# Optimization experiments

Measured on AMD Instinct MI355X. Metric: run time of the kernel, lower is better.

Reference implementation:

```python
import jax, jax.numpy as jnp
import numpy as np


def _gru(ub, lengths, W_ih, W_hh, b_ih, b_hh, h0):
    # ub: [B,T,E] pooled basket sequence; emulates packed GRU + pad_packed:
    # hidden carries forward only while t < length; outputs are zero past length.
    B, T, E = ub.shape
    x_t = jnp.transpose(ub, (1, 0, 2))                      # [T,B,E]
    mask_t = (jnp.arange(T)[:, None] < lengths[None, :])    # [T,B]
    xg_t = x_t @ W_ih.T + b_ih                              # [T,B,3E] precompute input gates

    def step(h, inp):
        xg, m = inp                                         # [B,3E], [B]
        hg = h @ W_hh.T + b_hh                              # [B,3E]
        xr, xz, xn = jnp.split(xg, 3, axis=-1)
        hr, hz, hn = jnp.split(hg, 3, axis=-1)
        r = jax.nn.sigmoid(xr + hr)
        z = jax.nn.sigmoid(xz + hz)
        n = jnp.tanh(xn + r * hn)
        h_new = (1.0 - z) * n + z * h
        m = m[:, None]
        h_next = jnp.where(m, h_new, h)
        out = jnp.where(m, h_new, 0.0)                      # pad_packed pads with zeros
        return h_next, out

    h_last, outs = jax.lax.scan(step, h0[0], (xg_t, mask_t))
    dynamic_user = jnp.transpose(outs, (1, 0, 2))           # [B,T,E]
    return dynamic_user, h_last[None]                        # h_u: [1,B,E]


def setup_inputs() -> dict:
    key = jax.random.key(0)
    B, T, M, E, V = 256, 50, 20, 128, 100000
    ks = jax.random.split(key, 8)
    basket_sizes = jax.random.randint(ks[0], (B, T), 1, M + 1)
    item_ids = jax.random.randint(ks[1], (B, T, M), 1, V + 2)
    pos = jnp.arange(M)
    item_ids = jnp.where(pos[None, None, :] < basket_sizes[..., None], item_ids, 0)
    lengths = jnp.sort(jax.random.randint(ks[2], (B,), 1, T + 1))[::-1]  # descending, like pack_padded
    emb = jax.random.normal(ks[3], (V + 2, E), jnp.float32) * 0.1
    emb = emb.at[0].set(0.0)                                 # padding_idx=0
    s = 1.0 / np.sqrt(E)
    W_ih = jax.random.uniform(ks[4], (3 * E, E), jnp.float32, -s, s)
    W_hh = jax.random.uniform(ks[5], (3 * E, E), jnp.float32, -s, s)
    b_ih = jax.random.uniform(ks[6], (3 * E,), jnp.float32, -s, s)
    b_hh = jax.random.uniform(ks[7], (3 * E,), jnp.float32, -s, s)
    h0 = jnp.zeros((1, B, E), jnp.float32)
    return {"item_ids": item_ids, "basket_sizes": basket_sizes, "lengths": lengths,
            "emb": emb, "W_ih": W_ih, "W_hh": W_hh, "b_ih": b_ih, "b_hh": b_hh, "h0": h0}


def reference(item_ids, basket_sizes, lengths, emb, W_ih, W_hh, b_ih, b_hh, h0):
    # Fused ragged embedding-bag (avg): row 0 of emb is zero, so padded slots
    # contribute nothing; divide by true basket size -> exact avg pool over basket.
    gathered = emb[item_ids]                                 # [B,T,M,E]
    ub_seqs = gathered.sum(axis=2) / basket_sizes[..., None].astype(gathered.dtype)  # [B,T,E]
    dynamic_user, h_u = _gru(ub_seqs, lengths, W_ih, W_hh, b_ih, b_hh, h0)
    return dynamic_user, h_u
```

## Files before the change

### kernel.cpp

```cpp
#include <hip/hip_runtime.h>
#include <stdint.h>

#define Bn 256
#define Tn 50
#define Mn 20
#define En 128
#define G3 384
#define MT 64
#define LDA 132

__device__ __forceinline__ float sigmoidf(float x) {
    return 1.0f / (1.0f + __expf(-x));
}
__device__ __forceinline__ float tanh_safe(float a) {
    float ax = fabsf(a);
    float e2 = __expf(-2.0f * ax);
    return copysignf((1.0f - e2) / (1.0f + e2), a);
}

__global__ __launch_bounds__(256) void gather_kernel(
    const int*   __restrict__ item_ids,
    const int*   __restrict__ basket_sizes,
    const float* __restrict__ emb,
    float* __restrict__ ub)
{
    const int bt   = blockIdx.x * 8 + (threadIdx.x >> 5);
    const int lane = threadIdx.x & 31;
    const int* ids = item_ids + (size_t)bt * Mn;
    float ax = 0.f, ay = 0.f, az = 0.f, aw = 0.f;
    #pragma unroll
    for (int m = 0; m < Mn; ++m) {
        const float4 v = *(const float4*)(emb + (size_t)ids[m] * En + lane * 4);
        ax += v.x; ay += v.y; az += v.z; aw += v.w;
    }
    const float inv = 1.0f / (float)basket_sizes[bt];
    *(float4*)(ub + (size_t)bt * En + lane * 4) =
        make_float4(ax * inv, ay * inv, az * inv, aw * inv);
}

__global__ __launch_bounds__(256, 2) void gemm_kernel(
    const float* __restrict__ ub,
    const float* __restrict__ W_ih,
    const float* __restrict__ b_ih,
    float* __restrict__ xg)
{
    __shared__ float A[MT][LDA];
    __shared__ float Bt[64][LDA];

    const int tid  = threadIdx.x;
    const int mt   = blockIdx.x / 6;
    const int nc   = blockIdx.x % 6;
    const int row0 = mt * MT;
    const int col0 = nc * 64;

    {
        const int r = tid >> 2, seg = tid & 3;
        const float4* srcA = (const float4*)(ub + (size_t)(row0 + r) * En + seg * 32);
        const float4* srcB = (const float4*)(W_ih + (size_t)(col0 + r) * En + seg * 32);
        float4* dstA = (float4*)&A[r][seg * 32];
        float4* dstB = (float4*)&Bt[r][seg * 32];
        #pragma unroll
        for (int c = 0; c < 8; ++c) { dstA[c] = srcA[c]; dstB[c] = srcB[c]; }
    }
    __syncthreads();

    const int tx = tid & 15;
    const int ty = tid >> 4;

    float acc[4][4];
    #pragma unroll
    for (int i = 0; i < 4; ++i)
        #pragma unroll
        for (int u = 0; u < 4; ++u) acc[i][u] = 0.0f;

    #pragma unroll 4
    for (int k4 = 0; k4 < 32; ++k4) {
        const float4 av[4] = {
            *(const float4*)&A[ty +  0][k4*4], *(const float4*)&A[ty + 16][k4*4],
            *(const float4*)&A[ty + 32][k4*4], *(const float4*)&A[ty + 48][k4*4]};
        const float4 bv[4] = {
            *(const float4*)&Bt[tx +  0][k4*4], *(const float4*)&Bt[tx + 16][k4*4],
            *(const float4*)&Bt[tx + 32][k4*4], *(const float4*)&Bt[tx + 48][k4*4]};
        #pragma unroll
        for (int i = 0; i < 4; ++i)
            #pragma unroll
            for (int u = 0; u < 4; ++u) {
                acc[i][u] = fmaf(av[i].x, bv[u].x, acc[i][u]);
                acc[i][u] = fmaf(av[i].y, bv[u].y, acc[i][u]);
                acc[i][u] = fmaf(av[i].z, bv[u].z, acc[i][u]);
                acc[i][u] = fmaf(av[i].w, bv[u].w, acc[i][u]);
            }
    }

    float bias[4];
    #pragma unroll
    for (int u = 0; u < 4; ++u) bias[u] = b_ih[col0 + tx + 16*u];
    #pragma unroll
    for (int i = 0; i < 4; ++i) {
        const size_t rowoff = (size_t)(row0 + ty + 16*i) * G3;
        #pragma unroll
        for (int u = 0; u < 4; ++u)
            xg[rowoff + col0 + tx + 16*u] = acc[i][u] + bias[u];
    }
}

__global__ __launch_bounds__(1024) void gru_kernel(
    const int*   __restrict__ lengths,
    const float* __restrict__ W_hh,
    const float* __restrict__ b_hh,
    const float* __restrict__ h0,
    const float* __restrict__ xg,
    float* __restrict__ out_dyn,
    float* __restrict__ out_h)
{
    __shared__ float hs[En];
    __shared__ float red[8][3][En];

    const int tid = threadIdx.x;
    const int b   = blockIdx.x;
    const int j   = tid & 127;
    const int q   = tid >> 7;

    float4 w0[4], w1[4], w2[4];
    {
        const float4* p0 = (const float4*)(W_hh + (size_t)(0*En + j) * En + q * 16);
        const float4* p1 = (const float4*)(W_hh + (size_t)(1*En + j) * En + q * 16);
        const float4* p2 = (const float4*)(W_hh + (size_t)(2*En + j) * En + q * 16);
        #pragma unroll
        for (int c = 0; c < 4; ++c) { w0[c] = p0[c]; w1[c] = p1[c]; w2[c] = p2[c]; }
    }

    const int len = lengths[b];
    const float* xgb = xg + (size_t)b * Tn * G3;
    float* outb = out_dyn + (size_t)b * Tn * En;

    float xr = 0.f, xz = 0.f, xn = 0.f, br = 0.f, bz = 0.f, bn = 0.f;
    if (tid < En) {
        hs[tid] = h0[(size_t)b * En + tid];
        br = b_hh[tid]; bz = b_hh[En + tid]; bn = b_hh[2*En + tid];
        xr = xgb[tid];  xz = xgb[En + tid]; xn = xgb[2*En + tid];
    }
    __syncthreads();

    for (int t = 0; t < len; ++t) {
        const float4* h4 = ((const float4*)hs) + q * 4;
        float a0 = 0.f, a1 = 0.f, a2 = 0.f;
        #pragma unroll
        for (int c = 0; c < 4; ++c) {
            const float4 hv = h4[c];
            a0 = fmaf(w0[c].x, hv.x, a0); a0 = fmaf(w0[c].y, hv.y, a0);
            a0 = fmaf(w0[c].z, hv.z, a0); a0 = fmaf(w0[c].w, hv.w, a0);
            a1 = fmaf(w1[c].x, hv.x, a1); a1 = fmaf(w1[c].y, hv.y, a1);
            a1 = fmaf(w1[c].z, hv.z, a1); a1 = fmaf(w1[c].w, hv.w, a1);
            a2 = fmaf(w2[c].x, hv.x, a2); a2 = fmaf(w2[c].y, hv.y, a2);
            a2 = fmaf(w2[c].z, hv.z, a2); a2 = fmaf(w2[c].w, hv.w, a2);
        }
        red[q][0][j] = a0; red[q][1][j] = a1; red[q][2][j] = a2;

        float nxr = 0.f, nxz = 0.f, nxn = 0.f;
        if (tid < En) {
            const int tn = (t + 1 < len) ? t + 1 : t;
            nxr = xgb[tn*G3 + tid];
            nxz = xgb[tn*G3 + En + tid];
            nxn = xgb[tn*G3 + 2*En + tid];
        }
        __syncthreads();

        if (tid < En) {
            float ar = red[0][0][tid], az = red[0][1][tid], an = red[0][2][tid];
            #pragma unroll
            for (int p = 1; p < 8; ++p) {
                ar += red[p][0][tid]; az += red[p][1][tid]; an += red[p][2][tid];
            }
            const float r = sigmoidf(xr + br + ar);
            const float z = sigmoidf(xz + bz + az);
            const float n = tanh_safe(xn + r * (bn + an));
            const float hnew = (1.0f - z) * n + z * hs[tid];
            hs[tid] = hnew;
            outb[t*En + tid] = hnew;
            xr = nxr; xz = nxz; xn = nxn;
        }
        __syncthreads();
    }

    if (tid < En) {
        for (int t = len; t < Tn; ++t) outb[t*En + tid] = 0.0f;
        out_h[(size_t)b * En + tid] = hs[tid];
    }
}

extern "C" void kernel_launch(void* const* d_in, const int* in_sizes, int n_in,
                              void* d_out, int out_size, void* d_ws, size_t ws_size,
                              hipStream_t stream) {
    const int*   item_ids     = (const int*)d_in[0];
    const int*   basket_sizes = (const int*)d_in[1];
    const int*   lengths      = (const int*)d_in[2];
    const float* emb          = (const float*)d_in[3];
    const float* W_ih         = (const float*)d_in[4];
    const float* W_hh         = (const float*)d_in[5];
    const float* b_ih         = (const float*)d_in[6];
    const float* b_hh         = (const float*)d_in[7];
    const float* h0           = (const float*)d_in[8];
    float* out = (float*)d_out;
    float* xg  = (float*)d_ws;
    float* ub  = out;

    gather_kernel<<<(Bn * Tn) / 8, 256, 0, stream>>>(item_ids, basket_sizes, emb, ub);
    gemm_kernel<<<1200, 256, 0, stream>>>(ub, W_ih, b_ih, xg);
    gru_kernel<<<Bn, 1024, 0, stream>>>(
        lengths, W_hh, b_hh, h0, xg, out, out + (size_t)Bn * Tn * En);
}
```

Before: 176.5 us.

## Restructure GRU recurrence to use shuffle reductions and double-buffered hidden state

The GRU kernel now uses 512 threads per batch row. Each group of 4 adjacent lanes splits the K dimension for one hidden unit and reduces with wavefront shuffles instead of shared-memory partial sums. The hidden state is double-buffered in shared memory, so each timestep needs one barrier instead of two. Gate math is computed redundantly by all 4 lanes, and the weight rows rotate their chunk order to reduce LDS bank conflicts. Each thread now holds twice as many weight registers (96 floats), which may pressure occupancy despite the launch bound of 2.

Result: no change. 176.5 us (+0.0%).

```diff
diff --git a/kernel.cpp b/kernel.cpp
--- a/kernel.cpp
+++ b/kernel.cpp
@@ -104,7 +104,7 @@
     }
 }
 
-__global__ __launch_bounds__(1024) void gru_kernel(
+__global__ __launch_bounds__(512, 2) void gru_kernel(
     const int*   __restrict__ lengths,
     const float* __restrict__ W_hh,
     const float* __restrict__ b_hh,
@@ -113,41 +113,42 @@
     float* __restrict__ out_dyn,
     float* __restrict__ out_h)
 {
-    __shared__ float hs[En];
-    __shared__ float red[8][3][En];
+    __shared__ float hs[2][En];
 
     const int tid = threadIdx.x;
     const int b   = blockIdx.x;
-    const int j   = tid & 127;
-    const int q   = tid >> 7;
-
-    float4 w0[4], w1[4], w2[4];
+    const int j   = tid >> 2;
+    const int q   = tid & 3;
+
+    float4 w0[8], w1[8], w2[8];
     {
-        const float4* p0 = (const float4*)(W_hh + (size_t)(0*En + j) * En + q * 16);
-        const float4* p1 = (const float4*)(W_hh + (size_t)(1*En + j) * En + q * 16);
-        const float4* p2 = (const float4*)(W_hh + (size_t)(2*En + j) * En + q * 16);
-        #pragma unroll
-        for (int c = 0; c < 4; ++c) { w0[c] = p0[c]; w1[c] = p1[c]; w2[c] = p2[c]; }
+        const float4* p0 = (const float4*)(W_hh + (size_t)(0*En + j) * En + q * 32);
+        const float4* p1 = (const float4*)(W_hh + (size_t)(1*En + j) * En + q * 32);
+        const float4* p2 = (const float4*)(W_hh + (size_t)(2*En + j) * En + q * 32);
+        #pragma unroll
+        for (int c = 0; c < 8; ++c) {
+            const int cc = (c + 2*q) & 7;
+            w0[c] = p0[cc]; w1[c] = p1[cc]; w2[c] = p2[cc];
+        }
     }
 
     const int len = lengths[b];
     const float* xgb = xg + (size_t)b * Tn * G3;
     float* outb = out_dyn + (size_t)b * Tn * En;
 
-    float xr = 0.f, xz = 0.f, xn = 0.f, br = 0.f, bz = 0.f, bn = 0.f;
-    if (tid < En) {
-        hs[tid] = h0[(size_t)b * En + tid];
-        br = b_hh[tid]; bz = b_hh[En + tid]; bn = b_hh[2*En + tid];
-        xr = xgb[tid];  xz = xgb[En + tid]; xn = xgb[2*En + tid];
-    }
+    const float br = b_hh[j], bz = b_hh[En + j], bn = b_hh[2*En + j];
+    float hprev = h0[(size_t)b * En + j];
+    if (q == 0) hs[0][j] = hprev;
+    float xr = xgb[j], xz = xgb[En + j], xn = xgb[2*En + j];
     __syncthreads();
 
+    int cur = 0;
     for (int t = 0; t < len; ++t) {
-        const float4* h4 = ((const float4*)hs) + q * 4;
+        const float4* h4 = ((const float4*)hs[cur]) + q * 8;
         float a0 = 0.f, a1 = 0.f, a2 = 0.f;
         #pragma unroll
-        for (int c = 0; c < 4; ++c) {
-            const float4 hv = h4[c];
+        for (int c = 0; c < 8; ++c) {
+            const float4 hv = h4[(c + 2*q) & 7];
             a0 = fmaf(w0[c].x, hv.x, a0); a0 = fmaf(w0[c].y, hv.y, a0);
             a0 = fmaf(w0[c].z, hv.z, a0); a0 = fmaf(w0[c].w, hv.w, a0);
             a1 = fmaf(w1[c].x, hv.x, a1); a1 = fmaf(w1[c].y, hv.y, a1);
@@ -155,37 +156,34 @@
             a2 = fmaf(w2[c].x, hv.x, a2); a2 = fmaf(w2[c].y, hv.y, a2);
             a2 = fmaf(w2[c].z, hv.z, a2); a2 = fmaf(w2[c].w, hv.w, a2);
         }
-        red[q][0][j] = a0; red[q][1][j] = a1; red[q][2][j] = a2;
-
-        float nxr = 0.f, nxz = 0.f, nxn = 0.f;
-        if (tid < En) {
-            const int tn = (t + 1 < len) ? t + 1 : t;
-            nxr = xgb[tn*G3 + tid];
-            nxz = xgb[tn*G3 + En + tid];
-            nxn = xgb[tn*G3 + 2*En + tid];
+
+        const int tn = (t + 1 < len) ? t + 1 : t;
+        const float nxr = xgb[tn*G3 + j];
+        const float nxz = xgb[tn*G3 + En + j];
+        const float nxn = xgb[tn*G3 + 2*En + j];
+
+        a0 += __shfl_xor(a0, 1); a0 += __shfl_xor(a0, 2);
+        a1 += __shfl_xor(a1, 1); a1 += __shfl_xor(a1, 2);
+        a2 += __shfl_xor(a2, 1); a2 += __shfl_xor(a2, 2);
+
+        const float r = sigmoidf(xr + br + a0);
+        const float z = sigmoidf(xz + bz + a1);
+        const float n = tanh_safe(xn + r * (bn + a2));
+        const float hnew = (1.0f - z) * n + z * hprev;
+
+        if (q == 0) {
+            hs[cur ^ 1][j] = hnew;
+            outb[t*En + j] = hnew;
         }
         __syncthreads();
-
-        if (tid < En) {
-            float ar = red[0][0][tid], az = red[0][1][tid], an = red[0][2][tid];
-            #pragma unroll
-            for (int p = 1; p < 8; ++p) {
-                ar += red[p][0][tid]; az += red[p][1][tid]; an += red[p][2][tid];
-            }
-            const float r = sigmoidf(xr + br + ar);
-            const float z = sigmoidf(xz + bz + az);
-            const float n = tanh_safe(xn + r * (bn + an));
-            const float hnew = (1.0f - z) * n + z * hs[tid];
-            hs[tid] = hnew;
-            outb[t*En + tid] = hnew;
-            xr = nxr; xz = nxz; xn = nxn;
-        }
-        __syncthreads();
-    }
-
-    if (tid < En) {
-        for (int t = len; t < Tn; ++t) outb[t*En + tid] = 0.0f;
-        out_h[(size_t)b * En + tid] = hs[tid];
+        hprev = hnew;
+        xr = nxr; xz = nxz; xn = nxn;
+        cur ^= 1;
+    }
+
+    if (q == 0) {
+        for (int t = len; t < Tn; ++t) outb[t*En + j] = 0.0f;
+        out_h[(size_t)b * En + j] = hprev;
     }
 }
 
@@ -207,6 +205,6 @@
 
     gather_kernel<<<(Bn * Tn) / 8, 256, 0, stream>>>(item_ids, basket_sizes, emb, ub);
     gemm_kernel<<<1200, 256, 0, stream>>>(ub, W_ih, b_ih, xg);
-    gru_kernel<<<Bn, 1024, 0, stream>>>(
+    gru_kernel<<<Bn, 512, 0, stream>>>(
         lengths, W_hh, b_hh, h0, xg, out, out + (size_t)Bn * Tn * En);
 }
```
